# Optimization experiments

Hardware: AMD Instinct MI355X
Metric: run time of the kernel (lower is better)

The kernel has to match this reference:

```python
import jax, jax.numpy as jnp
import numpy as np

N = 100000   # nodes
E = 1600000  # edges (node pairs)
D = 64       # msg_feature_len
H = 128      # hidden width of gate/message MLPs


def setup_inputs() -> dict:
    key = jax.random.key(0)
    ks = jax.random.split(key, 10)
    s = 0.05
    return {
        "node_weights": jax.random.uniform(ks[0], (N, 1), dtype=jnp.float32),
        "node_prev_features": jax.random.normal(ks[1], (N, D), dtype=jnp.float32),
        "self_idx": jax.random.randint(ks[2], (E,), 0, N),
        "neighbor_idx": jax.random.randint(ks[3], (E,), 0, N),
        "gw1": jax.random.normal(ks[4], (2 * D, H), dtype=jnp.float32) * s,
        "gb1": jnp.zeros((H,), jnp.float32),
        "gw2": jax.random.normal(ks[5], (H, 1), dtype=jnp.float32) * s,
        "gb2": jnp.zeros((1,), jnp.float32),
        "mw1": jax.random.normal(ks[6], (2 * D, H), dtype=jnp.float32) * s,
        "mb1": jnp.zeros((H,), jnp.float32),
        "mw2": jax.random.normal(ks[7], (H, D), dtype=jnp.float32) * s,
        "mb2": jnp.zeros((D,), jnp.float32),
        "pow_p": jax.random.normal(ks[8], (1,), dtype=jnp.float32),
    }


def reference(node_weights, node_prev_features, self_idx, neighbor_idx,
              gw1, gb1, gw2, gb2, mw1, mb1, mw2, mb2, pow_p):
    # gather + concat: message [E, 2D]
    msg = jnp.concatenate(
        [node_prev_features[self_idx], node_prev_features[neighbor_idx]], axis=1)
    w = node_weights[neighbor_idx]  # [E, 1]

    # gate MLP (Linear -> ReLU -> Linear): [E, 1]
    gate = jax.nn.relu(msg @ gw1 + gb1) @ gw2 + gb2
    # segment-softmax over edges grouped by self_idx, weighted by w**pow
    gmax = jax.ops.segment_max(gate, self_idx, num_segments=N)  # [N, 1]
    gate = (w ** pow_p) * jnp.exp(gate - gmax[self_idx])
    gsum = jax.ops.segment_sum(gate, self_idx, num_segments=N)  # [N, 1]
    gate = gate / (gsum[self_idx] + 1e-10)

    # message MLP: [E, D]
    x = jax.nn.relu(msg @ mw1 + mb1) @ mw2 + mb2

    # weighted scatter-sum back to nodes; single head -> mean is identity
    node_update = jax.ops.segment_sum(gate * x, self_idx, num_segments=N)
    return node_update + node_prev_features
```

## Files before the change

### kernel.cpp

```cpp
#include <hip/hip_runtime.h>
#include <hip/hip_bf16.h>

typedef __bf16 bf16x8 __attribute__((ext_vector_type(8)));
typedef float f32x4 __attribute__((ext_vector_type(4)));
typedef float f32x2 __attribute__((ext_vector_type(2)));

#define WIN 64
#define TILE 112
#define CHUNK 7
#define LSTR 136
#define SCAN_BLK 1024
#define SENT 0x7f7f7f7f

__global__ void k_wconv(const float* __restrict__ gw1, const float* __restrict__ mw1,
                        const float* __restrict__ mw2,
                        __bf16* __restrict__ Bt, __bf16* __restrict__ mw2t,
                        int* __restrict__ hist, int* __restrict__ s_lo,
                        int* __restrict__ s_hi, int N, int NB)
{
    int i = blockIdx.x * 256 + threadIdx.x;
    if (i < 32768) {
        int c = i >> 6, k = i & 63;
        float v;
        if (c < 128)      v = gw1[k * 128 + c];
        else if (c < 256) v = gw1[(64 + k) * 128 + (c - 128)];
        else if (c < 384) v = mw1[k * 128 + (c - 256)];
        else              v = mw1[(64 + k) * 128 + (c - 384)];
        Bt[i] = (__bf16)v;
    } else if (i < 40960) {
        int j = i - 32768;
        int c = j >> 7, k = j & 127;
        mw2t[j] = (__bf16)mw2[k * 64 + c];
    }
    if (i < N) hist[i] = 0;
    if (i < NB) { s_lo[i] = SENT; s_hi[i] = 0; }
}

__global__ void __launch_bounds__(256, 4)
k_tab(const float* __restrict__ feat, const __bf16* __restrict__ Bt,
      const float* __restrict__ gb1, const float* __restrict__ mb1,
      const int* __restrict__ selfi, int* __restrict__ hist,
      __bf16* __restrict__ Tp, unsigned char* __restrict__ Tq, int N, int E)
{
    for (int e = blockIdx.x * 256 + threadIdx.x; e < E; e += gridDim.x * 256)
        atomicAdd(&hist[selfi[e]], 1);

    const int tid = threadIdx.x;
    const int lane = tid & 63, wv = tid >> 6;
    const int la = lane & 15, kg = lane >> 4;
    const int r0 = blockIdx.x * 16;
    if (r0 >= N) return;

    bf16x8 a[2];
    #pragma unroll
    for (int kk = 0; kk < 2; ++kk) {
        const int rr = min(r0 + la, N - 1);
        const float* src = feat + (size_t)rr * 64 + kk * 32 + kg * 8;
        f32x4 f0 = *reinterpret_cast<const f32x4*>(src);
        f32x4 f1 = *reinterpret_cast<const f32x4*>(src + 4);
        #pragma unroll
        for (int j = 0; j < 4; ++j) { a[kk][j] = (__bf16)f0[j]; a[kk][4 + j] = (__bf16)f1[j]; }
    }
    #pragma unroll
    for (int j = 0; j < 8; ++j) {
        const int c = wv * 128 + j * 16 + la;
        float bias = 0.f;
        if (c < 128) bias = gb1[c];
        else if (c >= 256 && c < 384) bias = mb1[c - 256];
        f32x4 acc = {bias, bias, bias, bias};
        #pragma unroll
        for (int kk = 0; kk < 2; ++kk) {
            bf16x8 bb = *reinterpret_cast<const bf16x8*>(Bt + (size_t)c * 64 + kk * 32 + kg * 8);
            acc = __builtin_amdgcn_mfma_f32_16x16x32_bf16(a[kk], bb, acc, 0, 0, 0);
        }
        #pragma unroll
        for (int i = 0; i < 4; ++i) {
            const int row = r0 + kg * 4 + i;
            if (row < N) {
                if (c < 128) {
                    Tp[(size_t)row * 256 + c] = (__bf16)acc[i];
                } else if (c < 256) {
                    const int qc = c - 128;
                    const int pk = __builtin_amdgcn_cvt_pk_fp8_f32(acc[i], acc[i], 0, false);
                    Tq[(size_t)row * 256 + (qc >> 3) * 16 + (qc & 7)] = (unsigned char)(pk & 0xff);
                } else if (c < 384) {
                    Tp[(size_t)row * 256 + 128 + (c - 256)] = (__bf16)acc[i];
                } else {
                    const int qc = c - 384;
                    const int pk = __builtin_amdgcn_cvt_pk_fp8_f32(acc[i], acc[i], 0, false);
                    Tq[(size_t)row * 256 + (qc >> 3) * 16 + 8 + (qc & 7)] = (unsigned char)(pk & 0xff);
                }
            }
        }
    }
}

__global__ void k_scan1(const int* __restrict__ hist, int* __restrict__ incl,
                        int* __restrict__ bsum, int N)
{
    __shared__ int sd[SCAN_BLK];
    int i = blockIdx.x * SCAN_BLK + threadIdx.x;
    int v = (i < N) ? hist[i] : 0;
    sd[threadIdx.x] = v;
    __syncthreads();
    for (int off = 1; off < SCAN_BLK; off <<= 1) {
        int t = (threadIdx.x >= off) ? sd[threadIdx.x - off] : 0;
        __syncthreads();
        sd[threadIdx.x] += t;
        __syncthreads();
    }
    if (i < N) incl[i] = sd[threadIdx.x];
    if (threadIdx.x == SCAN_BLK - 1) bsum[blockIdx.x] = sd[SCAN_BLK - 1];
}

__global__ void k_scanb(const int* __restrict__ bsum, int* __restrict__ boff, int nb)
{
    __shared__ int sd[256];
    const int t = threadIdx.x;
    int v = (t < nb) ? bsum[t] : 0;
    sd[t] = v;
    __syncthreads();
    for (int off = 1; off < 256; off <<= 1) {
        int u = (t >= off) ? sd[t - off] : 0;
        __syncthreads();
        sd[t] += u;
        __syncthreads();
    }
    if (t < nb) boff[t] = sd[t] - v;
}

__global__ void k_scan23(const int* __restrict__ incl, const int* __restrict__ hist,
                         const int* __restrict__ boff,
                         int* __restrict__ cursor, int* __restrict__ starts,
                         int* __restrict__ s_lo, int* __restrict__ s_hi,
                         float* __restrict__ lpw, const float* __restrict__ nodew,
                         const float* __restrict__ powp,
                         const float* __restrict__ prev, float* __restrict__ out,
                         int N, int E)
{
    int i = blockIdx.x * SCAN_BLK + threadIdx.x;
    if (i >= N) return;
    const int h = hist[i];
    const int v = incl[i] - h + boff[blockIdx.x];
    cursor[i] = v;
    starts[i] = v;
    lpw[i] = powp[0] * __logf(nodew[i]);
    if (h > 0) {
        const int b = v / WIN;
        atomicMin(&s_lo[b], i);
        atomicMax(&s_hi[b], i + 1);
    } else {
        const float* ps = prev + (size_t)i * 64;
        float* po = out + (size_t)i * 64;
        for (int k = 0; k < 64; ++k) po[k] = ps[k];
    }
}

__global__ void k_scatter(const int* __restrict__ selfi, const int* __restrict__ nbri,
                          int* __restrict__ cursor, int* __restrict__ nbr_p, int E)
{
    int e = blockIdx.x * 256 + threadIdx.x;
    if (e >= E) return;
    int s = selfi[e];
    int pos = atomicAdd(&cursor[s], 1);
    nbr_p[pos] = nbri[e];
}

__global__ void __launch_bounds__(256, 5)
k_fused(const __bf16* __restrict__ Tp, const unsigned char* __restrict__ Tq,
        const int* __restrict__ nbr_p, const int* __restrict__ starts,
        const int* __restrict__ s_lo, const int* __restrict__ s_hi,
        const float* __restrict__ lpw,
        const float* __restrict__ gw2, const float* __restrict__ gb2,
        const __bf16* __restrict__ mw2t, const float* __restrict__ mb2,
        const float* __restrict__ prev, float* __restrict__ out,
        int N, int E)
{
    __shared__ __align__(16) __bf16 hlds[TILE][LSTR];
    __shared__ float logit_s[TILE];
    __shared__ float ginv_s[WIN];
    __shared__ int st_s[WIN + 1];

    const int b = blockIdx.x;
    const int s0 = s_lo[b];
    if (s0 == SENT) return;
    const int s1 = s_hi[b];
    const int nseg = s1 - s0;
    const int e0 = starts[s0];
    const int e1 = (s1 < N) ? starts[s1] : E;
    int ne = e1 - e0;
    if (ne > TILE) ne = TILE;

    const int tid = threadIdx.x;
    for (int j = tid; j <= nseg; j += 256)
        st_s[j] = (j < nseg) ? starts[s0 + j] : e1;
    __syncthreads();

    const int lane = tid & 63, wv = tid >> 6;
    const int g16 = tid >> 4, il = tid & 15;

    {
        const float b2v = gb2[0];
        float w2f[8];
        {
            f32x4 wa = *reinterpret_cast<const f32x4*>(gw2 + il * 8);
            f32x4 wb = *reinterpret_cast<const f32x4*>(gw2 + il * 8 + 4);
            w2f[0] = wa[0]; w2f[1] = wa[1]; w2f[2] = wa[2]; w2f[3] = wa[3];
            w2f[4] = wb[0]; w2f[5] = wb[1]; w2f[6] = wb[2]; w2f[7] = wb[3];
        }
        const int ck = (ne + 15) >> 4;
        const int rb = g16 * ck;
        const int re = min(rb + ck, ne);
        if (rb < re) {
            uint4 qv[CHUNK];
            float lpv[CHUNK];
            #pragma unroll
            for (int j = 0; j < CHUNK; ++j) {
                if (rb + j < re) {
                    const int nn = nbr_p[e0 + rb + j];
                    qv[j] = *reinterpret_cast<const uint4*>(Tq + (size_t)nn * 256 + il * 16);
                    lpv[j] = lpw[nn];
                }
            }
            int cur;
            {
                int lo = 0, hi = nseg - 1;
                while (lo < hi) {
                    const int mid = (lo + hi + 1) >> 1;
                    if (st_s[mid] <= e0 + rb) lo = mid; else hi = mid - 1;
                }
                cur = lo;
            }
            int curlim = st_s[cur + 1];
            float pgf[8], pmf[8];
            {
                const __bf16* tp = Tp + (size_t)(s0 + cur) * 256 + il * 8;
                bf16x8 pg = *reinterpret_cast<const bf16x8*>(tp);
                bf16x8 pm = *reinterpret_cast<const bf16x8*>(tp + 128);
                #pragma unroll
                for (int j = 0; j < 8; ++j) { pgf[j] = (float)pg[j]; pmf[j] = (float)pm[j]; }
            }
            #pragma unroll
            for (int j = 0; j < CHUNK; ++j) {
                if (rb + j < re) {
                    const int r = rb + j;
                    if (e0 + r >= curlim) {
                        do { ++cur; curlim = st_s[cur + 1]; } while (e0 + r >= curlim);
                        const __bf16* tp = Tp + (size_t)(s0 + cur) * 256 + il * 8;
                        bf16x8 pg = *reinterpret_cast<const bf16x8*>(tp);
                        bf16x8 pm = *reinterpret_cast<const bf16x8*>(tp + 128);
                        #pragma unroll
                        for (int q = 0; q < 8; ++q) { pgf[q] = (float)pg[q]; pmf[q] = (float)pm[q]; }
                    }
                    f32x2 g01 = __builtin_amdgcn_cvt_pk_f32_fp8(qv[j].x, false);
                    f32x2 g23 = __builtin_amdgcn_cvt_pk_f32_fp8(qv[j].x, true);
                    f32x2 g45 = __builtin_amdgcn_cvt_pk_f32_fp8(qv[j].y, false);
                    f32x2 g67 = __builtin_amdgcn_cvt_pk_f32_fp8(qv[j].y, true);
                    f32x2 m01 = __builtin_amdgcn_cvt_pk_f32_fp8(qv[j].z, false);
                    f32x2 m23 = __builtin_amdgcn_cvt_pk_f32_fp8(qv[j].z, true);
                    f32x2 m45 = __builtin_amdgcn_cvt_pk_f32_fp8(qv[j].w, false);
                    f32x2 m67 = __builtin_amdgcn_cvt_pk_f32_fp8(qv[j].w, true);
                    float qgv[8] = {g01[0], g01[1], g23[0], g23[1], g45[0], g45[1], g67[0], g67[1]};
                    float qmv[8] = {m01[0], m01[1], m23[0], m23[1], m45[0], m45[1], m67[0], m67[1]};
                    float lg = 0.f;
                    bf16x8 hv;
                    #pragma unroll
                    for (int q = 0; q < 8; ++q) {
                        lg = fmaf(fmaxf(pgf[q] + qgv[q], 0.f), w2f[q], lg);
                        hv[q] = (__bf16)fmaxf(pmf[q] + qmv[q], 0.f);
                    }
                    *reinterpret_cast<bf16x8*>(&hlds[r][il * 8]) = hv;
                    #pragma unroll
                    for (int sh = 1; sh < 16; sh <<= 1)
                        lg += __shfl_xor(lg, sh, 16);
                    if (il == 0) logit_s[r] = lg + b2v + lpv[j];
                }
            }
        }
    }
    __syncthreads();

    const int la = lane & 15, kg = lane >> 4;
    const int row0[2] = {wv * 16, 64 + wv * 16};
    const bool lv[2] = {row0[0] < ne, (wv < 3) && (row0[1] < ne)};

    f32x4 c2[2][4] = {};
    #pragma unroll
    for (int kk = 0; kk < 4; ++kk) {
        const int kbase = kk * 32 + kg * 8;
        bf16x8 a[2];
        #pragma unroll
        for (int m = 0; m < 2; ++m)
            if (lv[m]) a[m] = *reinterpret_cast<const bf16x8*>(&hlds[row0[m] + la][kbase]);
        #pragma unroll
        for (int n = 0; n < 4; ++n) {
            bf16x8 bb = *reinterpret_cast<const bf16x8*>(mw2t + (size_t)(n * 16 + la) * 128 + kbase);
            #pragma unroll
            for (int m = 0; m < 2; ++m)
                if (lv[m]) c2[m][n] = __builtin_amdgcn_mfma_f32_16x16x32_bf16(a[m], bb, c2[m][n], 0, 0, 0);
        }
    }

    for (int j = g16; j < nseg; j += 16) {
        int a0 = st_s[j] - e0;
        int a1 = st_s[j + 1] - e0;
        if (a1 > ne) a1 = ne;
        float mx = -3.4e38f;
        for (int idx = a0 + il; idx < a1; idx += 16)
            mx = fmaxf(mx, logit_s[idx]);
        #pragma unroll
        for (int sh = 1; sh < 16; sh <<= 1)
            mx = fmaxf(mx, __shfl_xor(mx, sh, 16));
        float sum = 0.f;
        for (int idx = a0 + il; idx < a1; idx += 16) {
            const float g = __expf(logit_s[idx] - mx);
            logit_s[idx] = g;
            sum += g;
        }
        #pragma unroll
        for (int sh = 1; sh < 16; sh <<= 1)
            sum += __shfl_xor(sum, sh, 16);
        if (il == 0) ginv_s[j] = 1.f / (sum + 1e-10f);
    }
    __syncthreads();

    float (*xb)[68] = reinterpret_cast<float(*)[68]>(&hlds[0][0]);
    #pragma unroll
    for (int m = 0; m < 2; ++m) {
        if (!lv[m]) continue;
        float cf[4];
        #pragma unroll
        for (int i = 0; i < 4; ++i) {
            const int row = row0[m] + kg * 4 + i;
            cf[i] = (row < ne) ? logit_s[row] : 0.f;
        }
        #pragma unroll
        for (int n = 0; n < 4; ++n) {
            const float b2v = mb2[n * 16 + la];
            #pragma unroll
            for (int i = 0; i < 4; ++i)
                xb[row0[m] + kg * 4 + i][n * 16 + la] = cf[i] * (c2[m][n][i] + b2v);
        }
    }
    __syncthreads();

    for (int j = wv; j < nseg; j += 4) {
        int a0 = st_s[j] - e0;
        int a1 = st_s[j + 1] - e0;
        if (a1 > ne) a1 = ne;
        if (a1 <= a0) continue;
        float sum = 0.f;
        for (int r = a0; r < a1; ++r) sum += xb[r][lane];
        const float gi = ginv_s[j];
        const size_t o = (size_t)(s0 + j) * 64 + lane;
        out[o] = prev[o] + sum * gi;
    }
}

extern "C" void kernel_launch(void* const* d_in, const int* in_sizes, int n_in,
                              void* d_out, int out_size, void* d_ws, size_t ws_size,
                              hipStream_t stream)
{
    const float* node_w = (const float*)d_in[0];
    const float* prev   = (const float*)d_in[1];
    const int*   selfi  = (const int*)d_in[2];
    const int*   nbri   = (const int*)d_in[3];
    const float* gw1 = (const float*)d_in[4];
    const float* gb1 = (const float*)d_in[5];
    const float* gw2 = (const float*)d_in[6];
    const float* gb2 = (const float*)d_in[7];
    const float* mw1 = (const float*)d_in[8];
    const float* mb1 = (const float*)d_in[9];
    const float* mw2 = (const float*)d_in[10];
    const float* mb2 = (const float*)d_in[11];
    const float* powp = (const float*)d_in[12];
    const int N = in_sizes[0];
    const int E = in_sizes[2];
    float* out = (float*)d_out;
    const int NB = (E + WIN - 1) / WIN;

    char* ws = (char*)d_ws;
    size_t off = 0;
    auto alloc = [&](size_t bytes) {
        void* p = ws + off;
        off = (off + bytes + 255) & ~(size_t)255;
        return p;
    };
    __bf16* Tp           = (__bf16*)alloc((size_t)N * 256 * 2);
    unsigned char* Tq    = (unsigned char*)alloc((size_t)N * 256);
    __bf16* Bt           = (__bf16*)alloc(512 * 64 * 2);
    __bf16* mw2t         = (__bf16*)alloc(64 * 128 * 2);
    int* nbr_p           = (int*)alloc((size_t)E * 4);
    int* hist            = (int*)alloc((size_t)N * 4);
    int* cursor          = (int*)alloc((size_t)N * 4);
    int* starts          = (int*)alloc((size_t)N * 4);
    int* incl            = (int*)alloc((size_t)N * 4);
    float* lpw           = (float*)alloc((size_t)N * 4);
    int* s_lo            = (int*)alloc((size_t)NB * 4);
    int* s_hi            = (int*)alloc((size_t)NB * 4);
    const int nb = (N + SCAN_BLK - 1) / SCAN_BLK;
    int* bsum            = (int*)alloc((size_t)nb * 4);
    int* boff            = (int*)alloc((size_t)nb * 4);

    int initN = N;
    if (initN < 40960) initN = 40960;
    if (initN < NB) initN = NB;
    k_wconv<<<(initN + 255) / 256, 256, 0, stream>>>(gw1, mw1, mw2, Bt, mw2t,
                                                     hist, s_lo, s_hi, N, NB);
    k_tab<<<(N + 15) / 16, 256, 0, stream>>>(prev, Bt, gb1, mb1, selfi, hist, Tp, Tq, N, E);
    k_scan1<<<nb, SCAN_BLK, 0, stream>>>(hist, incl, bsum, N);
    k_scanb<<<1, 256, 0, stream>>>(bsum, boff, nb);
    k_scan23<<<nb, SCAN_BLK, 0, stream>>>(incl, hist, boff, cursor, starts, s_lo, s_hi,
                                          lpw, node_w, powp, prev, out, N, E);
    k_scatter<<<(E + 255) / 256, 256, 0, stream>>>(selfi, nbri, cursor, nbr_p, E);
    k_fused<<<NB, 256, 0, stream>>>(Tp, Tq, nbr_p, starts, s_lo, s_hi, lpw,
                                    gw2, gb2, mw2t, mb2, prev, out, N, E);
}
```

Measured before the change: 504.9 us.

## Store self-side projection table in fp8 and stage table writes through LDS

The self-side precomputed table Tp changes from bf16 to fp8 with the same interleaved layout as Tq, which halves its footprint and the bytes each segment reload pulls in. k_tab now stages both tables in shared memory and writes them out as coalesced 16-byte rows instead of scattered single-byte and bf16 stores. The gather loop in k_fused also loads unconditionally, clamping out-of-range rows to the last valid edge, so loads can be issued without branches. The cost is lower precision in the self-side preactivations, which may shift the output numerically.

```diff
diff --git a/kernel.cpp b/kernel.cpp
--- a/kernel.cpp
+++ b/kernel.cpp
@@ -11,6 +11,15 @@
 #define LSTR 136
 #define SCAN_BLK 1024
 #define SENT 0x7f7f7f7f
+
+static __device__ __forceinline__ void dec8(unsigned x, unsigned y, float* o) {
+    f32x2 a = __builtin_amdgcn_cvt_pk_f32_fp8(x, false);
+    f32x2 b = __builtin_amdgcn_cvt_pk_f32_fp8(x, true);
+    f32x2 c = __builtin_amdgcn_cvt_pk_f32_fp8(y, false);
+    f32x2 d = __builtin_amdgcn_cvt_pk_f32_fp8(y, true);
+    o[0] = a[0]; o[1] = a[1]; o[2] = b[0]; o[3] = b[1];
+    o[4] = c[0]; o[5] = c[1]; o[6] = d[0]; o[7] = d[1];
+}
 
 __global__ void k_wconv(const float* __restrict__ gw1, const float* __restrict__ mw1,
                         const float* __restrict__ mw2,
@@ -40,8 +49,10 @@
 k_tab(const float* __restrict__ feat, const __bf16* __restrict__ Bt,
       const float* __restrict__ gb1, const float* __restrict__ mb1,
       const int* __restrict__ selfi, int* __restrict__ hist,
-      __bf16* __restrict__ Tp, unsigned char* __restrict__ Tq, int N, int E)
-{
+      unsigned char* __restrict__ Tp, unsigned char* __restrict__ Tq, int N, int E)
+{
+    __shared__ unsigned char ldsT[2][16][256];
+
     for (int e = blockIdx.x * 256 + threadIdx.x; e < E; e += gridDim.x * 256)
         atomicAdd(&hist[selfi[e]], 1);
 
@@ -73,24 +84,25 @@
             bf16x8 bb = *reinterpret_cast<const bf16x8*>(Bt + (size_t)c * 64 + kk * 32 + kg * 8);
             acc = __builtin_amdgcn_mfma_f32_16x16x32_bf16(a[kk], bb, acc, 0, 0, 0);
         }
+        int tbl, boff;
+        if (c < 128)      { tbl = 0; boff = ((c) >> 3) * 16 + (c & 7); }
+        else if (c < 256) { const int q = c - 128; tbl = 1; boff = (q >> 3) * 16 + (q & 7); }
+        else if (c < 384) { const int q = c - 256; tbl = 0; boff = (q >> 3) * 16 + 8 + (q & 7); }
+        else              { const int q = c - 384; tbl = 1; boff = (q >> 3) * 16 + 8 + (q & 7); }
         #pragma unroll
         for (int i = 0; i < 4; ++i) {
-            const int row = r0 + kg * 4 + i;
-            if (row < N) {
-                if (c < 128) {
-                    Tp[(size_t)row * 256 + c] = (__bf16)acc[i];
-                } else if (c < 256) {
-                    const int qc = c - 128;
-                    const int pk = __builtin_amdgcn_cvt_pk_fp8_f32(acc[i], acc[i], 0, false);
-                    Tq[(size_t)row * 256 + (qc >> 3) * 16 + (qc & 7)] = (unsigned char)(pk & 0xff);
-                } else if (c < 384) {
-                    Tp[(size_t)row * 256 + 128 + (c - 256)] = (__bf16)acc[i];
-                } else {
-                    const int qc = c - 384;
-                    const int pk = __builtin_amdgcn_cvt_pk_fp8_f32(acc[i], acc[i], 0, false);
-                    Tq[(size_t)row * 256 + (qc >> 3) * 16 + 8 + (qc & 7)] = (unsigned char)(pk & 0xff);
-                }
-            }
+            const int pk = __builtin_amdgcn_cvt_pk_fp8_f32(acc[i], acc[i], 0, false);
+            ldsT[tbl][kg * 4 + i][boff] = (unsigned char)(pk & 0xff);
+        }
+    }
+    __syncthreads();
+    {
+        const int row = tid >> 4, v4 = tid & 15;
+        if (r0 + row < N) {
+            const uint4* s0p = reinterpret_cast<const uint4*>(&ldsT[0][row][0]);
+            const uint4* s1p = reinterpret_cast<const uint4*>(&ldsT[1][row][0]);
+            reinterpret_cast<uint4*>(Tp + (size_t)(r0 + row) * 256)[v4] = s0p[v4];
+            reinterpret_cast<uint4*>(Tq + (size_t)(r0 + row) * 256)[v4] = s1p[v4];
         }
     }
 }
@@ -167,7 +179,7 @@
 }
 
 __global__ void __launch_bounds__(256, 5)
-k_fused(const __bf16* __restrict__ Tp, const unsigned char* __restrict__ Tq,
+k_fused(const unsigned char* __restrict__ Tp, const unsigned char* __restrict__ Tq,
         const int* __restrict__ nbr_p, const int* __restrict__ starts,
         const int* __restrict__ s_lo, const int* __restrict__ s_hi,
         const float* __restrict__ lpw,
@@ -211,16 +223,16 @@
         const int ck = (ne + 15) >> 4;
         const int rb = g16 * ck;
         const int re = min(rb + ck, ne);
-        if (rb < re) {
+        const int m = re - rb;
+        if (m > 0) {
             uint4 qv[CHUNK];
             float lpv[CHUNK];
             #pragma unroll
             for (int j = 0; j < CHUNK; ++j) {
-                if (rb + j < re) {
-                    const int nn = nbr_p[e0 + rb + j];
-                    qv[j] = *reinterpret_cast<const uint4*>(Tq + (size_t)nn * 256 + il * 16);
-                    lpv[j] = lpw[nn];
-                }
+                const int rc = (j < m) ? (rb + j) : (re - 1);
+                const int nn = nbr_p[e0 + rc];
+                qv[j] = *reinterpret_cast<const uint4*>(Tq + (size_t)nn * 256 + il * 16);
+                lpv[j] = lpw[nn];
             }
             int cur;
             {
@@ -234,34 +246,23 @@
             int curlim = st_s[cur + 1];
             float pgf[8], pmf[8];
             {
-                const __bf16* tp = Tp + (size_t)(s0 + cur) * 256 + il * 8;
-                bf16x8 pg = *reinterpret_cast<const bf16x8*>(tp);
-                bf16x8 pm = *reinterpret_cast<const bf16x8*>(tp + 128);
-                #pragma unroll
-                for (int j = 0; j < 8; ++j) { pgf[j] = (float)pg[j]; pmf[j] = (float)pm[j]; }
+                const uint4 tpv = *reinterpret_cast<const uint4*>(Tp + (size_t)(s0 + cur) * 256 + il * 16);
+                dec8(tpv.x, tpv.y, pgf);
+                dec8(tpv.z, tpv.w, pmf);
             }
             #pragma unroll
             for (int j = 0; j < CHUNK; ++j) {
-                if (rb + j < re) {
+                if (j < m) {
                     const int r = rb + j;
                     if (e0 + r >= curlim) {
                         do { ++cur; curlim = st_s[cur + 1]; } while (e0 + r >= curlim);
-                        const __bf16* tp = Tp + (size_t)(s0 + cur) * 256 + il * 8;
-                        bf16x8 pg = *reinterpret_cast<const bf16x8*>(tp);
-                        bf16x8 pm = *reinterpret_cast<const bf16x8*>(tp + 128);
-                        #pragma unroll
-                        for (int q = 0; q < 8; ++q) { pgf[q] = (float)pg[q]; pmf[q] = (float)pm[q]; }
+                        const uint4 tpv = *reinterpret_cast<const uint4*>(Tp + (size_t)(s0 + cur) * 256 + il * 16);
+                        dec8(tpv.x, tpv.y, pgf);
+                        dec8(tpv.z, tpv.w, pmf);
                     }
-                    f32x2 g01 = __builtin_amdgcn_cvt_pk_f32_fp8(qv[j].x, false);
-                    f32x2 g23 = __builtin_amdgcn_cvt_pk_f32_fp8(qv[j].x, true);
-                    f32x2 g45 = __builtin_amdgcn_cvt_pk_f32_fp8(qv[j].y, false);
-                    f32x2 g67 = __builtin_amdgcn_cvt_pk_f32_fp8(qv[j].y, true);
-                    f32x2 m01 = __builtin_amdgcn_cvt_pk_f32_fp8(qv[j].z, false);
-                    f32x2 m23 = __builtin_amdgcn_cvt_pk_f32_fp8(qv[j].z, true);
-                    f32x2 m45 = __builtin_amdgcn_cvt_pk_f32_fp8(qv[j].w, false);
-                    f32x2 m67 = __builtin_amdgcn_cvt_pk_f32_fp8(qv[j].w, true);
-                    float qgv[8] = {g01[0], g01[1], g23[0], g23[1], g45[0], g45[1], g67[0], g67[1]};
-                    float qmv[8] = {m01[0], m01[1], m23[0], m23[1], m45[0], m45[1], m67[0], m67[1]};
+                    float qgv[8], qmv[8];
+                    dec8(qv[j].x, qv[j].y, qgv);
+                    dec8(qv[j].z, qv[j].w, qmv);
                     float lg = 0.f;
                     bf16x8 hv;
                     #pragma unroll
@@ -386,7 +387,7 @@
         off = (off + bytes + 255) & ~(size_t)255;
         return p;
     };
-    __bf16* Tp           = (__bf16*)alloc((size_t)N * 256 * 2);
+    unsigned char* Tp    = (unsigned char*)alloc((size_t)N * 256);
     unsigned char* Tq    = (unsigned char*)alloc((size_t)N * 256);
     __bf16* Bt           = (__bf16*)alloc(512 * 64 * 2);
     __bf16* mw2t         = (__bf16*)alloc(64 * 128 * 2);
```

After: 481.7 us. 4.6% less time.
